# Optimization experiments

Measured on AMD Instinct MI355X. Metric: run time of the kernel, lower is better.

## Reference

```python
import jax, jax.numpy as jnp
import numpy as np

B, D_IN = 16384, 1024
N_DOM, EMB = 4, 16
H1, H2, H3 = 512, 256, 128
FH = 64
EPS = 1e-5


def setup_inputs() -> dict:
    key = jax.random.key(0)
    ks = jax.random.split(key, 32)
    s = 0.02
    def rn(k, shape):
        return jax.random.normal(k, shape, dtype=jnp.float32) * s
    inp = {
        "x": jax.random.normal(ks[0], (B, D_IN), dtype=jnp.float32),
        "domain_ids": jax.random.randint(ks[1], (B,), 0, N_DOM),
        # PartitionedNormalization params
        "pn_w": jnp.ones((N_DOM, D_IN), jnp.float32),
        "pn_b": jnp.zeros((N_DOM, D_IN), jnp.float32),
        # center net: D_IN->512->256->128
        "cW1": rn(ks[2], (D_IN, H1)), "cb1": jnp.zeros((H1,), jnp.float32),
        "cW2": rn(ks[3], (H1, H2)),  "cb2": jnp.zeros((H2,), jnp.float32),
        "cW3": rn(ks[4], (H2, H3)),  "cb3": jnp.zeros((H3,), jnp.float32),
        # domain-specific nets, stacked over domains
        "dW1": rn(ks[5], (N_DOM, D_IN, H1)), "db1": jnp.zeros((N_DOM, H1), jnp.float32),
        "dW2": rn(ks[6], (N_DOM, H1, H2)),  "db2": jnp.zeros((N_DOM, H2), jnp.float32),
        "dW3": rn(ks[7], (N_DOM, H2, H3)),  "db3": jnp.full((N_DOM, H3), 1.0, jnp.float32),  # domain_net_init_bias=1.0
        # final mlp: 128->64->1
        "fW1": rn(ks[8], (H3, FH)), "fb1": jnp.zeros((FH,), jnp.float32),
        "fW2": rn(ks[9], (FH, 1)),  "fb2": jnp.zeros((1,), jnp.float32),
        # domain embedding + auxiliary net: 16->32->1
        "dom_emb": rn(ks[10], (N_DOM, EMB)),
        "aW1": rn(ks[11], (EMB, 32)), "ab1": jnp.zeros((32,), jnp.float32),
        "aW2": rn(ks[12], (32, 1)),   "ab2": jnp.zeros((1,), jnp.float32),
    }
    return inp


def _forward(x, domain_ids, pn_w, pn_b,
             cW1, cb1, cW2, cb2, cW3, cb3,
             dW1, db1, dW2, db2, dW3, db3,
             fW1, fb1, fW2, fb2,
             dom_emb, aW1, ab1, aW2, ab2):
    # Partitioned normalization: per-sample layernorm over features,
    # domain-conditional affine (vectorized gather instead of python loop)
    mean = jnp.mean(x, axis=1, keepdims=True)
    var = jnp.mean(jnp.square(x - mean), axis=1, keepdims=True)  # unbiased=False
    norm = (x - mean) / jnp.sqrt(var + EPS)
    norm = norm * pn_w[domain_ids] + pn_b[domain_ids]  # (B, D_IN)

    # center net
    h = jax.nn.relu(norm @ cW1 + cb1)
    h = jax.nn.relu(h @ cW2 + cb2)
    h_center = h @ cW3 + cb3  # (B, H3)

    # domain-specific nets: compute all domains, then gather per-sample
    hd = jax.nn.relu(jnp.einsum('bi,dio->bdo', norm, dW1) + db1[None])   # (B,D,H1)
    hd = jax.nn.relu(jnp.einsum('bdi,dio->bdo', hd, dW2) + db2[None])    # (B,D,H2)
    hd = jnp.einsum('bdi,dio->bdo', hd, dW3) + db3[None]                 # (B,D,H3)
    h_domain = jnp.take_along_axis(hd, domain_ids[:, None, None], axis=1)[:, 0]  # (B,H3)

    h_fused = h_center * jnp.tanh(h_domain)

    main = jax.nn.relu(h_fused @ fW1 + fb1) @ fW2 + fb2  # (B,1)

    de = dom_emb[domain_ids]                              # (B,EMB)
    aux = jax.nn.relu(de @ aW1 + ab1) @ aW2 + ab2         # (B,1)

    return jax.nn.sigmoid(main + aux)


def reference(x, domain_ids, pn_w, pn_b,
              cW1, cb1, cW2, cb2, cW3, cb3,
              dW1, db1, dW2, db2, dW3, db3,
              fW1, fb1, fW2, fb2,
              dom_emb, aW1, ab1, aW2, ab2):
    return _forward(x, domain_ids, pn_w, pn_b,
                    cW1, cb1, cW2, cb2, cW3, cb3,
                    dW1, db1, dW2, db2, dW3, db3,
                    fW1, fb1, fW2, fb2,
                    dom_emb, aW1, ab1, aW2, ab2)
```

## Files before the change

kernel.cpp:

```cpp
#include <hip/hip_runtime.h>
#include <hip/hip_bf16.h>
#include <stdint.h>

#define NB   16384
#define DIN  1024
#define MPAD 16896

typedef __bf16 bf16;
typedef __bf16 v8bf __attribute__((ext_vector_type(8)));
typedef float  v4f  __attribute__((ext_vector_type(4)));

typedef __attribute__((address_space(1))) void* as1_ptr;
typedef __attribute__((address_space(3))) void* as3_ptr;

__device__ __forceinline__ void gl_lds16(const void* g, void* l) {
  __builtin_amdgcn_global_load_lds((as1_ptr)(g), (as3_ptr)(l), 16, 0, 0);
}

__device__ __forceinline__ unsigned short bfbits(float f) {
  bf16 h = (bf16)f;
  return __builtin_bit_cast(unsigned short, h);
}

__global__ __launch_bounds__(1024) void k_histscan_aux(
    const int* __restrict__ dom, int* __restrict__ pstart, int* __restrict__ cnt2,
    int* __restrict__ perm, float* __restrict__ aux,
    const float* __restrict__ dom_emb, const float* __restrict__ aW1,
    const float* __restrict__ ab1, const float* __restrict__ aW2,
    const float* __restrict__ ab2) {
  __shared__ int hist[4];
  int tid = threadIdx.x, lane = tid & 63;
  if (tid < 4) hist[tid] = 0;
  if (tid >= 8 && tid < 12) cnt2[tid - 8] = 0;
  for (int j = tid; j < MPAD; j += 1024) perm[j] = -1;
  __syncthreads();
  int c0 = 0, c1 = 0, c2 = 0, c3 = 0;
#pragma unroll
  for (int it = 0; it < 16; it++) {
    int d = dom[it * 1024 + tid];
    c0 += (d == 0); c1 += (d == 1); c2 += (d == 2); c3 += (d == 3);
  }
#pragma unroll
  for (int o = 32; o; o >>= 1) {
    c0 += __shfl_xor(c0, o, 64); c1 += __shfl_xor(c1, o, 64);
    c2 += __shfl_xor(c2, o, 64); c3 += __shfl_xor(c3, o, 64);
  }
  if (lane == 0) {
    atomicAdd(&hist[0], c0); atomicAdd(&hist[1], c1);
    atomicAdd(&hist[2], c2); atomicAdd(&hist[3], c3);
  }
  __syncthreads();
  if (tid == 0) {
    int p = 0;
    for (int d = 0; d < 4; d++) { pstart[d] = p; p += (hist[d] + 127) & ~127; }
    pstart[4] = p;
  }
  if (tid < 4) {
    float a = ab2[0];
    for (int j = 0; j < 32; j++) {
      float s = ab1[j];
      for (int i = 0; i < 16; i++) s += dom_emb[tid * 16 + i] * aW1[i * 32 + j];
      a += fmaxf(s, 0.f) * aW2[j];
    }
    aux[tid] = a;
  }
}

__global__ void k_assign(const int* __restrict__ dom, const int* __restrict__ pstart,
                         int* __restrict__ cnt2, int* __restrict__ perm,
                         int* __restrict__ rowpos) {
  int i = blockIdx.x * 256 + threadIdx.x;
  int lane = threadIdx.x & 63;
  int d = dom[i];
  unsigned long long ltmask = (1ull << lane) - 1ull;
#pragma unroll
  for (int dd = 0; dd < 4; dd++) {
    unsigned long long m = __ballot(d == dd);
    int c = __popcll(m);
    int base = 0;
    if (lane == 0 && c) base = atomicAdd(&cnt2[dd], c);
    base = __shfl(base, 0, 64);
    if (d == dd) {
      int pos = pstart[dd] + base + __popcll(m & ltmask);
      perm[pos] = i;
      rowpos[i] = pos;
    }
  }
}

__global__ __launch_bounds__(256) void k_ln(const float* __restrict__ x,
                                            const int* __restrict__ dom,
                                            const int* __restrict__ rowpos,
                                            const float* __restrict__ pn_w,
                                            const float* __restrict__ pn_b,
                                            bf16* __restrict__ norm) {
  int wv = threadIdx.x >> 6, lane = threadIdx.x & 63;
  int r = blockIdx.x * 4 + wv;
  const float* xr = x + (size_t)r * DIN;
  float4 v[4];
#pragma unroll
  for (int g = 0; g < 4; g++) v[g] = *(const float4*)(xr + g * 256 + lane * 4);
  float s = 0.f;
#pragma unroll
  for (int g = 0; g < 4; g++) s += v[g].x + v[g].y + v[g].z + v[g].w;
#pragma unroll
  for (int o = 32; o; o >>= 1) s += __shfl_xor(s, o, 64);
  float mean = s * (1.f / 1024.f);
  float q = 0.f;
#pragma unroll
  for (int g = 0; g < 4; g++) {
    float a = v[g].x - mean, b = v[g].y - mean, c = v[g].z - mean, e = v[g].w - mean;
    q += a * a + b * b + c * c + e * e;
  }
#pragma unroll
  for (int o = 32; o; o >>= 1) q += __shfl_xor(q, o, 64);
  float rstd = rsqrtf(q * (1.f / 1024.f) + 1e-5f);
  int d = dom[r];
  int pos = rowpos[r];
  const float* pw = pn_w + (size_t)d * DIN;
  const float* pb = pn_b + (size_t)d * DIN;
  bf16* orow = norm + (size_t)pos * DIN;
#pragma unroll
  for (int g = 0; g < 4; g++) {
    float4 w4 = *(const float4*)(pw + g * 256 + lane * 4);
    float4 b4 = *(const float4*)(pb + g * 256 + lane * 4);
    ushort4 o;
    o.x = bfbits((v[g].x - mean) * rstd * w4.x + b4.x);
    o.y = bfbits((v[g].y - mean) * rstd * w4.y + b4.y);
    o.z = bfbits((v[g].z - mean) * rstd * w4.z + b4.z);
    o.w = bfbits((v[g].w - mean) * rstd * w4.w + b4.w);
    *(ushort4*)(orow + g * 256 + lane * 4) = o;
  }
}

__global__ __launch_bounds__(256) void k_wt_all(
    const float* __restrict__ cW1, const float* __restrict__ cW2,
    const float* __restrict__ cW3, const float* __restrict__ dW1,
    const float* __restrict__ dW2, const float* __restrict__ dW3,
    const float* __restrict__ fW1,
    bf16* __restrict__ cW1t, bf16* __restrict__ cW2t, bf16* __restrict__ cW3t,
    bf16* __restrict__ dW1t, bf16* __restrict__ dW2t, bf16* __restrict__ dW3t,
    bf16* __restrict__ fW1t) {
  __shared__ float t[64 * 65];
  int bid = blockIdx.x;
  const float* src; bf16* dst; int K, N, tile;
  if (bid < 640) {
    K = 1024; N = 512; int m = bid >> 7; tile = bid & 127;
    src = m == 0 ? cW1 : dW1 + (size_t)(m - 1) * 524288;
    dst = m == 0 ? cW1t : dW1t + (size_t)(m - 1) * 524288;
  } else if (bid < 800) {
    K = 512; N = 256; int m = (bid - 640) >> 5; tile = (bid - 640) & 31;
    src = m == 0 ? cW2 : dW2 + (size_t)(m - 1) * 131072;
    dst = m == 0 ? cW2t : dW2t + (size_t)(m - 1) * 131072;
  } else if (bid < 840) {
    K = 256; N = 128; int m = (bid - 800) >> 3; tile = (bid - 800) & 7;
    src = m == 0 ? cW3 : dW3 + (size_t)(m - 1) * 32768;
    dst = m == 0 ? cW3t : dW3t + (size_t)(m - 1) * 32768;
  } else {
    K = 128; N = 64; tile = bid - 840;
    src = fW1; dst = fW1t;
  }
  int ntn = N >> 6;
  int k0 = (tile / ntn) << 6, n0 = (tile % ntn) << 6;
  int tid = threadIdx.x;
  int r = tid >> 2, c4 = (tid & 3) << 4;
#pragma unroll
  for (int j4 = 0; j4 < 4; j4++) {
    float4 v = *(const float4*)(src + (size_t)(k0 + r) * N + n0 + c4 + j4 * 4);
    t[r * 65 + c4 + j4 * 4 + 0] = v.x;
    t[r * 65 + c4 + j4 * 4 + 1] = v.y;
    t[r * 65 + c4 + j4 * 4 + 2] = v.z;
    t[r * 65 + c4 + j4 * 4 + 3] = v.w;
  }
  __syncthreads();
  int n = tid >> 2, kc = (tid & 3) << 4;
#pragma unroll
  for (int j4 = 0; j4 < 4; j4++) {
    ushort4 o;
    o.x = bfbits(t[(kc + j4 * 4 + 0) * 65 + n]);
    o.y = bfbits(t[(kc + j4 * 4 + 1) * 65 + n]);
    o.z = bfbits(t[(kc + j4 * 4 + 2) * 65 + n]);
    o.w = bfbits(t[(kc + j4 * 4 + 3) * 65 + n]);
    *(ushort4*)(dst + (size_t)(n0 + n) * K + k0 + kc + j4 * 4) = o;
  }
}

__global__ __launch_bounds__(256) void k_gemm(const bf16* __restrict__ A, int lda,
                                              int aoffc, int aoffd,
                                              const bf16* __restrict__ cWt,
                                              const bf16* __restrict__ dWt,
                                              const float* __restrict__ cb,
                                              const float* __restrict__ db,
                                              bf16* __restrict__ C, int Nh, int Kd,
                                              int relu, const int* __restrict__ pstart,
                                              int lognct) {
  __shared__ bf16 Al[128 * 64];
  __shared__ bf16 Bl[128 * 64];
  const int tid = threadIdx.x;
  const int wv = tid >> 6, lane = tid & 63;
  const int nct = 1 << lognct;
  const int T1 = nct << 7;
  int l = blockIdx.x, rt, ct;
  if (l < T1) {
    int t = l >> 3;
    ct = t & (nct - 1);
    rt = ((t >> lognct) << 3) | (l & 7);
  } else {
    int l2 = l - T1;
    rt = 128 + (l2 >> lognct);
    ct = l2 & (nct - 1);
  }
  const int row0 = rt * 128;
  int d = 0;
  if (row0 >= pstart[1]) d = 1;
  if (row0 >= pstart[2]) d = 2;
  if (row0 >= pstart[3]) d = 3;
  const int n0 = ct * 128;
  const bool isd = (n0 >= Nh);
  const bf16* Wt = isd ? dWt + ((size_t)d * Nh + (n0 - Nh)) * Kd : cWt + (size_t)n0 * Kd;
  const float* bias = isd ? db + d * Nh + (n0 - Nh) : cb + n0;
  const int aoff = isd ? aoffd : aoffc;
  const bf16* Ab = A + (size_t)row0 * lda + aoff;

  v4f acc[4][4];
#pragma unroll
  for (int i = 0; i < 4; i++)
#pragma unroll
    for (int j = 0; j < 4; j++) acc[i][j] = v4f{0.f, 0.f, 0.f, 0.f};

  const int wm = (wv >> 1) * 64, wn = (wv & 1) * 64;
  const int mrow = lane & 15, quad = lane >> 4;
  const int lrow = lane >> 3;
  const int lchk = lane & 7;
  const int ldc = 2 * Nh;

  for (int kt = 0; kt < Kd; kt += 64) {
#pragma unroll
    for (int p = 0; p < 4; p++) {
      int rbase = wv * 32 + p * 8;
      int r = rbase + lrow;
      int jg = lchk ^ (r & 7);
      gl_lds16(Ab + (size_t)r * lda + kt + jg * 8, &Al[rbase * 64]);
      gl_lds16(Wt + (size_t)r * Kd + kt + jg * 8, &Bl[rbase * 64]);
    }
    __syncthreads();
#pragma unroll
    for (int s = 0; s < 2; s++) {
      v8bf af[4], bfr[4];
#pragma unroll
      for (int mi = 0; mi < 4; mi++) {
        int m = wm + mi * 16 + mrow;
        int j = (s * 4 + quad) ^ (m & 7);
        af[mi] = *(const v8bf*)&Al[m * 64 + j * 8];
      }
#pragma unroll
      for (int ni = 0; ni < 4; ni++) {
        int n = wn + ni * 16 + mrow;
        int j = (s * 4 + quad) ^ (n & 7);
        bfr[ni] = *(const v8bf*)&Bl[n * 64 + j * 8];
      }
#pragma unroll
      for (int mi = 0; mi < 4; mi++)
#pragma unroll
        for (int ni = 0; ni < 4; ni++)
          acc[mi][ni] =
              __builtin_amdgcn_mfma_f32_16x16x32_bf16(af[mi], bfr[ni], acc[mi][ni], 0, 0, 0);
    }
    __syncthreads();
  }

  float bv[4];
#pragma unroll
  for (int ni = 0; ni < 4; ni++) bv[ni] = bias[wn + ni * 16 + mrow];
#pragma unroll
  for (int mi = 0; mi < 4; mi++) {
    int growb = row0 + wm + mi * 16 + quad * 4;
#pragma unroll
    for (int ni = 0; ni < 4; ni++) {
      int gcol = n0 + wn + ni * 16 + mrow;
#pragma unroll
      for (int r2 = 0; r2 < 4; r2++) {
        float v = acc[mi][ni][r2] + bv[ni];
        if (relu) v = fmaxf(v, 0.f);
        C[(size_t)(growb + r2) * ldc + gcol] = (bf16)v;
      }
    }
  }
}

__global__ __launch_bounds__(256) void k_gemm3(const bf16* __restrict__ A,
                                               const bf16* __restrict__ cW3t,
                                               const bf16* __restrict__ dW3t,
                                               const float* __restrict__ cb3,
                                               const float* __restrict__ db3,
                                               const bf16* __restrict__ fW1t,
                                               const float* __restrict__ fb1,
                                               const float* __restrict__ fW2,
                                               const float* __restrict__ fb2,
                                               const int* __restrict__ perm,
                                               const int* __restrict__ pstart,
                                               const float* __restrict__ aux,
                                               float* __restrict__ out) {
  __shared__ __align__(16) bf16 Al[64 * 64];
  __shared__ __align__(16) bf16 Bl[128 * 64];
  __shared__ __align__(16) bf16 fusedL[64 * 128];
  __shared__ __align__(16) bf16 fwB[64 * 128];
  const int tid = threadIdx.x, wv = tid >> 6, lane = tid & 63;
  const int row0 = blockIdx.x * 64;
  const int d = (row0 >= pstart[1]) + (row0 >= pstart[2]) + (row0 >= pstart[3]);
  const bf16* Ab = A + (size_t)row0 * 512;
  const int mrow = lane & 15, quad = lane >> 4, lrow = lane >> 3, lchk = lane & 7;
  const int wm = (wv >> 1) * 32, wn = (wv & 1) * 64;

  {
    int c = lane & 15, rsub = lane >> 4;
#pragma unroll
    for (int p = 0; p < 1; p++) {
      int rbase = wv * 16 + p * 4 * 4;
      (void)rbase;
    }
#pragma unroll
    for (int p = 0; p < 4; p++) {
      int rbase = wv * 16 + p * 4;
      int row = rbase + rsub;
      int g = (c & 8) | ((c ^ row) & 7);
      gl_lds16(fW1t + row * 128 + g * 8, &fwB[rbase * 128]);
    }
  }

  v4f accC[2][4], accD[2][4];
#pragma unroll
  for (int i = 0; i < 2; i++)
#pragma unroll
    for (int j = 0; j < 4; j++) { accC[i][j] = v4f{0.f,0.f,0.f,0.f}; accD[i][j] = v4f{0.f,0.f,0.f,0.f}; }

#pragma unroll
  for (int ph = 0; ph < 2; ph++) {
    const bf16* Wt = ph ? dW3t + (size_t)d * 32768 : cW3t;
    const int aoff = ph * 256;
    for (int kt = 0; kt < 256; kt += 64) {
#pragma unroll
      for (int p = 0; p < 2; p++) {
        int rbase = wv * 16 + p * 8;
        int r = rbase + lrow;
        int jg = lchk ^ (r & 7);
        gl_lds16(Ab + (size_t)r * 512 + aoff + kt + jg * 8, &Al[rbase * 64]);
      }
#pragma unroll
      for (int p = 0; p < 4; p++) {
        int rbase = wv * 32 + p * 8;
        int r = rbase + lrow;
        int jg = lchk ^ (r & 7);
        gl_lds16(Wt + (size_t)r * 256 + kt + jg * 8, &Bl[rbase * 64]);
      }
      __syncthreads();
#pragma unroll
      for (int s = 0; s < 2; s++) {
        v8bf af[2], bfr[4];
#pragma unroll
        for (int mi = 0; mi < 2; mi++) {
          int m = wm + mi * 16 + mrow;
          int j = (s * 4 + quad) ^ (m & 7);
          af[mi] = *(const v8bf*)&Al[m * 64 + j * 8];
        }
#pragma unroll
        for (int ni = 0; ni < 4; ni++) {
          int n = wn + ni * 16 + mrow;
          int j = (s * 4 + quad) ^ (n & 7);
          bfr[ni] = *(const v8bf*)&Bl[n * 64 + j * 8];
        }
        if (ph == 0) {
#pragma unroll
          for (int mi = 0; mi < 2; mi++)
#pragma unroll
            for (int ni = 0; ni < 4; ni++)
              accC[mi][ni] = __builtin_amdgcn_mfma_f32_16x16x32_bf16(af[mi], bfr[ni], accC[mi][ni], 0, 0, 0);
        } else {
#pragma unroll
          for (int mi = 0; mi < 2; mi++)
#pragma unroll
            for (int ni = 0; ni < 4; ni++)
              accD[mi][ni] = __builtin_amdgcn_mfma_f32_16x16x32_bf16(af[mi], bfr[ni], accD[mi][ni], 0, 0, 0);
        }
      }
      __syncthreads();
    }
  }

#pragma unroll
  for (int mi = 0; mi < 2; mi++) {
    int rowb = wm + mi * 16 + quad * 4;
#pragma unroll
    for (int ni = 0; ni < 4; ni++) {
      int col = wn + ni * 16 + mrow;
      float cbv = cb3[col];
      float dbv = db3[d * 128 + col];
      int jc = col >> 3, coff = col & 7;
#pragma unroll
      for (int r2 = 0; r2 < 4; r2++) {
        int rr = rowb + r2;
        float f = (accC[mi][ni][r2] + cbv) * tanhf(accD[mi][ni][r2] + dbv);
        int cs = (jc & 8) | ((jc ^ rr) & 7);
        fusedL[rr * 128 + cs * 8 + coff] = (bf16)f;
      }
    }
  }
  __syncthreads();

  float fb1v[4], fW2v[4];
#pragma unroll
  for (int nt = 0; nt < 4; nt++) {
    int col = nt * 16 + mrow;
    fb1v[nt] = fb1[col];
    fW2v[nt] = fW2[col];
  }
  v4f hacc[4];
#pragma unroll
  for (int nt = 0; nt < 4; nt++) hacc[nt] = v4f{0.f, 0.f, 0.f, 0.f};
  const int m = wv * 16 + mrow;
#pragma unroll
  for (int s = 0; s < 4; s++) {
    int j = s * 4 + quad;
    int ca = (j & 8) | ((j ^ m) & 7);
    v8bf af = *(const v8bf*)&fusedL[m * 128 + ca * 8];
#pragma unroll
    for (int nt = 0; nt < 4; nt++) {
      int n = nt * 16 + mrow;
      int cbk = (j & 8) | ((j ^ n) & 7);
      v8bf bfr = *(const v8bf*)&fwB[n * 128 + cbk * 8];
      hacc[nt] = __builtin_amdgcn_mfma_f32_16x16x32_bf16(af, bfr, hacc[nt], 0, 0, 0);
    }
  }
  float ys[4];
#pragma unroll
  for (int r2 = 0; r2 < 4; r2++) {
    float s = 0.f;
#pragma unroll
    for (int nt = 0; nt < 4; nt++) s += fmaxf(hacc[nt][r2] + fb1v[nt], 0.f) * fW2v[nt];
    ys[r2] = s;
  }
#pragma unroll
  for (int o = 1; o < 16; o <<= 1)
#pragma unroll
    for (int r2 = 0; r2 < 4; r2++) ys[r2] += __shfl_xor(ys[r2], o, 64);
  if (mrow == 0) {
    const float addc = fb2[0] + aux[d];
#pragma unroll
    for (int r2 = 0; r2 < 4; r2++) {
      int prow = row0 + wv * 16 + quad * 4 + r2;
      int orig = perm[prow];
      if (orig >= 0) out[orig] = 1.f / (1.f + expf(-(ys[r2] + addc)));
    }
  }
}

extern "C" void kernel_launch(void* const* d_in, const int* in_sizes, int n_in,
                              void* d_out, int out_size, void* d_ws, size_t ws_size,
                              hipStream_t stream) {
  (void)in_sizes; (void)n_in; (void)out_size; (void)ws_size;
  const float* x      = (const float*)d_in[0];
  const int*   dom    = (const int*)d_in[1];
  const float* pn_w   = (const float*)d_in[2];
  const float* pn_b   = (const float*)d_in[3];
  const float* cW1    = (const float*)d_in[4];
  const float* cb1    = (const float*)d_in[5];
  const float* cW2    = (const float*)d_in[6];
  const float* cb2    = (const float*)d_in[7];
  const float* cW3    = (const float*)d_in[8];
  const float* cb3    = (const float*)d_in[9];
  const float* dW1    = (const float*)d_in[10];
  const float* db1    = (const float*)d_in[11];
  const float* dW2    = (const float*)d_in[12];
  const float* db2    = (const float*)d_in[13];
  const float* dW3    = (const float*)d_in[14];
  const float* db3    = (const float*)d_in[15];
  const float* fW1    = (const float*)d_in[16];
  const float* fb1    = (const float*)d_in[17];
  const float* fW2    = (const float*)d_in[18];
  const float* fb2    = (const float*)d_in[19];
  const float* demb   = (const float*)d_in[20];
  const float* aW1    = (const float*)d_in[21];
  const float* ab1    = (const float*)d_in[22];
  const float* aW2    = (const float*)d_in[23];
  const float* ab2    = (const float*)d_in[24];
  float* out = (float*)d_out;

  char* w = (char*)d_ws;
  int*   cnt2   = (int*)(w + 16);
  int*   pstart = (int*)(w + 32);
  float* aux    = (float*)(w + 64);
  int*   perm   = (int*)(w + 256);
  int*   rowpos = (int*)(w + 67840);
  bf16*  bufA   = (bf16*)(w + 133376);
  bf16*  bufB   = (bf16*)(w + 34736384);
  bf16*  cW1t   = (bf16*)(w + 69339392);
  bf16*  cW2t   = (bf16*)(w + 70387968);
  bf16*  cW3t   = (bf16*)(w + 70650112);
  bf16*  dW1t   = (bf16*)(w + 70715648);
  bf16*  dW2t   = (bf16*)(w + 74909952);
  bf16*  dW3t   = (bf16*)(w + 75958528);
  bf16*  fW1t   = (bf16*)(w + 76220672);

  k_histscan_aux<<<1, 1024, 0, stream>>>(dom, pstart, cnt2, perm, aux,
                                         demb, aW1, ab1, aW2, ab2);
  k_assign<<<64, 256, 0, stream>>>(dom, pstart, cnt2, perm, rowpos);
  k_ln<<<4096, 256, 0, stream>>>(x, dom, rowpos, pn_w, pn_b, bufA);
  k_wt_all<<<842, 256, 0, stream>>>(cW1, cW2, cW3, dW1, dW2, dW3, fW1,
                                    cW1t, cW2t, cW3t, dW1t, dW2t, dW3t, fW1t);

  k_gemm<<<1056, 256, 0, stream>>>(bufA, 1024, 0, 0, cW1t, dW1t, cb1, db1,
                                   bufB, 512, 1024, 1, pstart, 3);
  k_gemm<<<528, 256, 0, stream>>>(bufB, 1024, 0, 512, cW2t, dW2t, cb2, db2,
                                  bufA, 256, 512, 1, pstart, 2);
  k_gemm3<<<264, 256, 0, stream>>>(bufA, cW3t, dW3t, cb3, db3, fW1t,
                                   fb1, fW2, fb2, perm, pstart, aux, out);
}
```

Before: 267.6 us.

## Switch activations and weights to FP8 MFMA and merge sort kernels

Converts normalized activations, intermediate hidden layers and the transposed weights from bf16 to fp8 (e4m3). Weights are scaled by 16 and outputs rescaled, and all three GEMM stages use fp8 MFMA, halving memory traffic and raising matrix throughput. Separately, the histogram and assignment kernels are merged into a single-block kernel using an LDS prefix scan, removing one launch and the atomics. The cost is much lower precision, which risks exceeding the accuracy tolerance.

Result: faster. 254.4 us (-4.9%).

```diff
diff --git a/kernel.cpp b/kernel.cpp
--- a/kernel.cpp
+++ b/kernel.cpp
@@ -9,6 +9,7 @@
 typedef __bf16 bf16;
 typedef __bf16 v8bf __attribute__((ext_vector_type(8)));
 typedef float  v4f  __attribute__((ext_vector_type(4)));
+typedef unsigned char u8;
 
 typedef __attribute__((address_space(1))) void* as1_ptr;
 typedef __attribute__((address_space(3))) void* as3_ptr;
@@ -22,38 +23,59 @@
   return __builtin_bit_cast(unsigned short, h);
 }
 
-__global__ __launch_bounds__(1024) void k_histscan_aux(
-    const int* __restrict__ dom, int* __restrict__ pstart, int* __restrict__ cnt2,
-    int* __restrict__ perm, float* __restrict__ aux,
+__device__ __forceinline__ unsigned short pk8(float a, float b) {
+  int u = __builtin_amdgcn_cvt_pk_fp8_f32(a, b, 0, false);
+  return (unsigned short)(u & 0xffff);
+}
+
+__global__ __launch_bounds__(1024) void k_sort(
+    const int* __restrict__ dom, int* __restrict__ pstart_g,
+    int* __restrict__ perm, int* __restrict__ rowpos, float* __restrict__ aux,
     const float* __restrict__ dom_emb, const float* __restrict__ aW1,
     const float* __restrict__ ab1, const float* __restrict__ aW2,
     const float* __restrict__ ab2) {
-  __shared__ int hist[4];
-  int tid = threadIdx.x, lane = tid & 63;
-  if (tid < 4) hist[tid] = 0;
-  if (tid >= 8 && tid < 12) cnt2[tid - 8] = 0;
+  __shared__ int sc0[1024], sc1[1024], sc2[1024], sc3[1024];
+  const int tid = threadIdx.x;
+  int dv[16];
+  int c0 = 0, c1 = 0, c2 = 0, c3 = 0;
+#pragma unroll
+  for (int it = 0; it < 16; it++) {
+    int d = dom[it * 1024 + tid];
+    dv[it] = d;
+    c0 += (d == 0); c1 += (d == 1); c2 += (d == 2); c3 += (d == 3);
+  }
+  sc0[tid] = c0; sc1[tid] = c1; sc2[tid] = c2; sc3[tid] = c3;
   for (int j = tid; j < MPAD; j += 1024) perm[j] = -1;
   __syncthreads();
-  int c0 = 0, c1 = 0, c2 = 0, c3 = 0;
+  for (int off = 1; off < 1024; off <<= 1) {
+    int v0 = (tid >= off) ? sc0[tid - off] : 0;
+    int v1 = (tid >= off) ? sc1[tid - off] : 0;
+    int v2 = (tid >= off) ? sc2[tid - off] : 0;
+    int v3 = (tid >= off) ? sc3[tid - off] : 0;
+    __syncthreads();
+    sc0[tid] += v0; sc1[tid] += v1; sc2[tid] += v2; sc3[tid] += v3;
+    __syncthreads();
+  }
+  const int t0 = sc0[1023], t1 = sc1[1023], t2 = sc2[1023];
+  const int s1 = (t0 + 127) & ~127;
+  const int s2 = s1 + ((t1 + 127) & ~127);
+  const int s3 = s2 + ((t2 + 127) & ~127);
+  int b0 = 0 + sc0[tid] - c0;
+  int b1 = s1 + sc1[tid] - c1;
+  int b2 = s2 + sc2[tid] - c2;
+  int b3 = s3 + sc3[tid] - c3;
 #pragma unroll
   for (int it = 0; it < 16; it++) {
-    int d = dom[it * 1024 + tid];
-    c0 += (d == 0); c1 += (d == 1); c2 += (d == 2); c3 += (d == 3);
-  }
-#pragma unroll
-  for (int o = 32; o; o >>= 1) {
-    c0 += __shfl_xor(c0, o, 64); c1 += __shfl_xor(c1, o, 64);
-    c2 += __shfl_xor(c2, o, 64); c3 += __shfl_xor(c3, o, 64);
-  }
-  if (lane == 0) {
-    atomicAdd(&hist[0], c0); atomicAdd(&hist[1], c1);
-    atomicAdd(&hist[2], c2); atomicAdd(&hist[3], c3);
-  }
-  __syncthreads();
+    int i = it * 1024 + tid;
+    int d = dv[it];
+    int pos = (d == 0) ? b0++ : ((d == 1) ? b1++ : ((d == 2) ? b2++ : b3++));
+    perm[pos] = i;
+    rowpos[i] = pos;
+  }
   if (tid == 0) {
-    int p = 0;
-    for (int d = 0; d < 4; d++) { pstart[d] = p; p += (hist[d] + 127) & ~127; }
-    pstart[4] = p;
+    int t3 = sc3[1023];
+    pstart_g[0] = 0; pstart_g[1] = s1; pstart_g[2] = s2; pstart_g[3] = s3;
+    pstart_g[4] = s3 + ((t3 + 127) & ~127);
   }
   if (tid < 4) {
     float a = ab2[0];
@@ -66,34 +88,12 @@
   }
 }
 
-__global__ void k_assign(const int* __restrict__ dom, const int* __restrict__ pstart,
-                         int* __restrict__ cnt2, int* __restrict__ perm,
-                         int* __restrict__ rowpos) {
-  int i = blockIdx.x * 256 + threadIdx.x;
-  int lane = threadIdx.x & 63;
-  int d = dom[i];
-  unsigned long long ltmask = (1ull << lane) - 1ull;
-#pragma unroll
-  for (int dd = 0; dd < 4; dd++) {
-    unsigned long long m = __ballot(d == dd);
-    int c = __popcll(m);
-    int base = 0;
-    if (lane == 0 && c) base = atomicAdd(&cnt2[dd], c);
-    base = __shfl(base, 0, 64);
-    if (d == dd) {
-      int pos = pstart[dd] + base + __popcll(m & ltmask);
-      perm[pos] = i;
-      rowpos[i] = pos;
-    }
-  }
-}
-
 __global__ __launch_bounds__(256) void k_ln(const float* __restrict__ x,
                                             const int* __restrict__ dom,
                                             const int* __restrict__ rowpos,
                                             const float* __restrict__ pn_w,
                                             const float* __restrict__ pn_b,
-                                            bf16* __restrict__ norm) {
+                                            u8* __restrict__ norm) {
   int wv = threadIdx.x >> 6, lane = threadIdx.x & 63;
   int r = blockIdx.x * 4 + wv;
   const float* xr = x + (size_t)r * DIN;
@@ -119,17 +119,18 @@
   int pos = rowpos[r];
   const float* pw = pn_w + (size_t)d * DIN;
   const float* pb = pn_b + (size_t)d * DIN;
-  bf16* orow = norm + (size_t)pos * DIN;
+  u8* orow = norm + (size_t)pos * DIN;
 #pragma unroll
   for (int g = 0; g < 4; g++) {
     float4 w4 = *(const float4*)(pw + g * 256 + lane * 4);
     float4 b4 = *(const float4*)(pb + g * 256 + lane * 4);
-    ushort4 o;
-    o.x = bfbits((v[g].x - mean) * rstd * w4.x + b4.x);
-    o.y = bfbits((v[g].y - mean) * rstd * w4.y + b4.y);
-    o.z = bfbits((v[g].z - mean) * rstd * w4.z + b4.z);
-    o.w = bfbits((v[g].w - mean) * rstd * w4.w + b4.w);
-    *(ushort4*)(orow + g * 256 + lane * 4) = o;
+    float f0 = (v[g].x - mean) * rstd * w4.x + b4.x;
+    float f1 = (v[g].y - mean) * rstd * w4.y + b4.y;
+    float f2 = (v[g].z - mean) * rstd * w4.z + b4.z;
+    float f3 = (v[g].w - mean) * rstd * w4.w + b4.w;
+    int u = __builtin_amdgcn_cvt_pk_fp8_f32(f0, f1, 0, false);
+    u = __builtin_amdgcn_cvt_pk_fp8_f32(f2, f3, u, true);
+    *(unsigned int*)(orow + g * 256 + lane * 4) = (unsigned int)u;
   }
 }
 
@@ -138,12 +139,12 @@
     const float* __restrict__ cW3, const float* __restrict__ dW1,
     const float* __restrict__ dW2, const float* __restrict__ dW3,
     const float* __restrict__ fW1,
-    bf16* __restrict__ cW1t, bf16* __restrict__ cW2t, bf16* __restrict__ cW3t,
-    bf16* __restrict__ dW1t, bf16* __restrict__ dW2t, bf16* __restrict__ dW3t,
+    u8* __restrict__ cW1t, u8* __restrict__ cW2t, u8* __restrict__ cW3t,
+    u8* __restrict__ dW1t, u8* __restrict__ dW2t, u8* __restrict__ dW3t,
     bf16* __restrict__ fW1t) {
   __shared__ float t[64 * 65];
   int bid = blockIdx.x;
-  const float* src; bf16* dst; int K, N, tile;
+  const float* src; u8* dst; int K, N, tile; bool isf = false;
   if (bid < 640) {
     K = 1024; N = 512; int m = bid >> 7; tile = bid & 127;
     src = m == 0 ? cW1 : dW1 + (size_t)(m - 1) * 524288;
@@ -157,8 +158,7 @@
     src = m == 0 ? cW3 : dW3 + (size_t)(m - 1) * 32768;
     dst = m == 0 ? cW3t : dW3t + (size_t)(m - 1) * 32768;
   } else {
-    K = 128; N = 64; tile = bid - 840;
-    src = fW1; dst = fW1t;
+    K = 128; N = 64; tile = bid - 840; src = fW1; dst = nullptr; isf = true;
   }
   int ntn = N >> 6;
   int k0 = (tile / ntn) << 6, n0 = (tile % ntn) << 6;
@@ -174,28 +174,41 @@
   }
   __syncthreads();
   int n = tid >> 2, kc = (tid & 3) << 4;
-#pragma unroll
-  for (int j4 = 0; j4 < 4; j4++) {
-    ushort4 o;
-    o.x = bfbits(t[(kc + j4 * 4 + 0) * 65 + n]);
-    o.y = bfbits(t[(kc + j4 * 4 + 1) * 65 + n]);
-    o.z = bfbits(t[(kc + j4 * 4 + 2) * 65 + n]);
-    o.w = bfbits(t[(kc + j4 * 4 + 3) * 65 + n]);
-    *(ushort4*)(dst + (size_t)(n0 + n) * K + k0 + kc + j4 * 4) = o;
-  }
-}
-
-__global__ __launch_bounds__(256) void k_gemm(const bf16* __restrict__ A, int lda,
+  if (!isf) {
+#pragma unroll
+    for (int j4 = 0; j4 < 4; j4++) {
+      float v0 = t[(kc + j4 * 4 + 0) * 65 + n] * 16.f;
+      float v1 = t[(kc + j4 * 4 + 1) * 65 + n] * 16.f;
+      float v2 = t[(kc + j4 * 4 + 2) * 65 + n] * 16.f;
+      float v3 = t[(kc + j4 * 4 + 3) * 65 + n] * 16.f;
+      int u = __builtin_amdgcn_cvt_pk_fp8_f32(v0, v1, 0, false);
+      u = __builtin_amdgcn_cvt_pk_fp8_f32(v2, v3, u, true);
+      *(unsigned int*)(dst + (size_t)(n0 + n) * K + k0 + kc + j4 * 4) = (unsigned int)u;
+    }
+  } else {
+#pragma unroll
+    for (int j4 = 0; j4 < 4; j4++) {
+      ushort4 o;
+      o.x = bfbits(t[(kc + j4 * 4 + 0) * 65 + n]);
+      o.y = bfbits(t[(kc + j4 * 4 + 1) * 65 + n]);
+      o.z = bfbits(t[(kc + j4 * 4 + 2) * 65 + n]);
+      o.w = bfbits(t[(kc + j4 * 4 + 3) * 65 + n]);
+      *(ushort4*)(fW1t + (size_t)(n0 + n) * K + k0 + kc + j4 * 4) = o;
+    }
+  }
+}
+
+__global__ __launch_bounds__(256) void k_gemm(const u8* __restrict__ A, int lda,
                                               int aoffc, int aoffd,
-                                              const bf16* __restrict__ cWt,
-                                              const bf16* __restrict__ dWt,
+                                              const u8* __restrict__ cWt,
+                                              const u8* __restrict__ dWt,
                                               const float* __restrict__ cb,
                                               const float* __restrict__ db,
-                                              bf16* __restrict__ C, int Nh, int Kd,
+                                              u8* __restrict__ C, int Nh, int Kd,
                                               int relu, const int* __restrict__ pstart,
                                               int lognct) {
-  __shared__ bf16 Al[128 * 64];
-  __shared__ bf16 Bl[128 * 64];
+  __shared__ __align__(16) u8 Al[128 * 64];
+  __shared__ __align__(16) u8 Bl[128 * 64];
   const int tid = threadIdx.x;
   const int wv = tid >> 6, lane = tid & 63;
   const int nct = 1 << lognct;
@@ -217,10 +230,10 @@
   if (row0 >= pstart[3]) d = 3;
   const int n0 = ct * 128;
   const bool isd = (n0 >= Nh);
-  const bf16* Wt = isd ? dWt + ((size_t)d * Nh + (n0 - Nh)) * Kd : cWt + (size_t)n0 * Kd;
+  const u8* Wt = isd ? dWt + ((size_t)d * Nh + (n0 - Nh)) * Kd : cWt + (size_t)n0 * Kd;
   const float* bias = isd ? db + d * Nh + (n0 - Nh) : cb + n0;
   const int aoff = isd ? aoffd : aoffc;
-  const bf16* Ab = A + (size_t)row0 * lda + aoff;
+  const u8* Ab = A + (size_t)row0 * lda + aoff;
 
   v4f acc[4][4];
 #pragma unroll
@@ -230,41 +243,43 @@
 
   const int wm = (wv >> 1) * 64, wn = (wv & 1) * 64;
   const int mrow = lane & 15, quad = lane >> 4;
-  const int lrow = lane >> 3;
-  const int lchk = lane & 7;
+  const int lrow = lane >> 2;
+  const int lchk = lane & 3;
   const int ldc = 2 * Nh;
 
   for (int kt = 0; kt < Kd; kt += 64) {
 #pragma unroll
-    for (int p = 0; p < 4; p++) {
-      int rbase = wv * 32 + p * 8;
+    for (int p = 0; p < 2; p++) {
+      int rbase = wv * 32 + p * 16;
       int r = rbase + lrow;
-      int jg = lchk ^ (r & 7);
-      gl_lds16(Ab + (size_t)r * lda + kt + jg * 8, &Al[rbase * 64]);
-      gl_lds16(Wt + (size_t)r * Kd + kt + jg * 8, &Bl[rbase * 64]);
+      int jg = lchk ^ (r & 3);
+      gl_lds16(Ab + (size_t)r * lda + kt + jg * 16, &Al[rbase * 64]);
+      gl_lds16(Wt + (size_t)r * Kd + kt + jg * 16, &Bl[rbase * 64]);
     }
     __syncthreads();
 #pragma unroll
     for (int s = 0; s < 2; s++) {
-      v8bf af[4], bfr[4];
+      long af[4], bfr[4];
 #pragma unroll
       for (int mi = 0; mi < 4; mi++) {
         int m = wm + mi * 16 + mrow;
-        int j = (s * 4 + quad) ^ (m & 7);
-        af[mi] = *(const v8bf*)&Al[m * 64 + j * 8];
+        int jc = s * 2 + (quad >> 1);
+        int js = jc ^ (m & 3);
+        af[mi] = *(const long*)&Al[m * 64 + js * 16 + (quad & 1) * 8];
       }
 #pragma unroll
       for (int ni = 0; ni < 4; ni++) {
         int n = wn + ni * 16 + mrow;
-        int j = (s * 4 + quad) ^ (n & 7);
-        bfr[ni] = *(const v8bf*)&Bl[n * 64 + j * 8];
+        int jc = s * 2 + (quad >> 1);
+        int js = jc ^ (n & 3);
+        bfr[ni] = *(const long*)&Bl[n * 64 + js * 16 + (quad & 1) * 8];
       }
 #pragma unroll
       for (int mi = 0; mi < 4; mi++)
 #pragma unroll
         for (int ni = 0; ni < 4; ni++)
           acc[mi][ni] =
-              __builtin_amdgcn_mfma_f32_16x16x32_bf16(af[mi], bfr[ni], acc[mi][ni], 0, 0, 0);
+              __builtin_amdgcn_mfma_f32_16x16x32_fp8_fp8(af[mi], bfr[ni], acc[mi][ni], 0, 0, 0);
     }
     __syncthreads();
   }
@@ -280,17 +295,19 @@
       int gcol = n0 + wn + ni * 16 + mrow;
 #pragma unroll
       for (int r2 = 0; r2 < 4; r2++) {
-        float v = acc[mi][ni][r2] + bv[ni];
+        float v = acc[mi][ni][r2] * 0.0625f + bv[ni];
         if (relu) v = fmaxf(v, 0.f);
-        C[(size_t)(growb + r2) * ldc + gcol] = (bf16)v;
-      }
-    }
-  }
-}
-
-__global__ __launch_bounds__(256) void k_gemm3(const bf16* __restrict__ A,
-                                               const bf16* __restrict__ cW3t,
-                                               const bf16* __restrict__ dW3t,
+        float g = __shfl_xor(v, 1, 64);
+        if (!(mrow & 1))
+          *(unsigned short*)(C + (size_t)(growb + r2) * ldc + gcol) = pk8(v, g);
+      }
+    }
+  }
+}
+
+__global__ __launch_bounds__(256) void k_gemm3(const u8* __restrict__ A,
+                                               const u8* __restrict__ cW3t,
+                                               const u8* __restrict__ dW3t,
                                                const float* __restrict__ cb3,
                                                const float* __restrict__ db3,
                                                const bf16* __restrict__ fW1t,
@@ -301,24 +318,20 @@
                                                const int* __restrict__ pstart,
                                                const float* __restrict__ aux,
                                                float* __restrict__ out) {
-  __shared__ __align__(16) bf16 Al[64 * 64];
-  __shared__ __align__(16) bf16 Bl[128 * 64];
+  __shared__ __align__(16) u8 Al[64 * 64];
+  __shared__ __align__(16) u8 Bl[128 * 64];
   __shared__ __align__(16) bf16 fusedL[64 * 128];
   __shared__ __align__(16) bf16 fwB[64 * 128];
   const int tid = threadIdx.x, wv = tid >> 6, lane = tid & 63;
   const int row0 = blockIdx.x * 64;
   const int d = (row0 >= pstart[1]) + (row0 >= pstart[2]) + (row0 >= pstart[3]);
-  const bf16* Ab = A + (size_t)row0 * 512;
-  const int mrow = lane & 15, quad = lane >> 4, lrow = lane >> 3, lchk = lane & 7;
+  const u8* Ab = A + (size_t)row0 * 512;
+  const int mrow = lane & 15, quad = lane >> 4;
+  const int lrow = lane >> 2, lchk = lane & 3;
   const int wm = (wv >> 1) * 32, wn = (wv & 1) * 64;
 
   {
     int c = lane & 15, rsub = lane >> 4;
-#pragma unroll
-    for (int p = 0; p < 1; p++) {
-      int rbase = wv * 16 + p * 4 * 4;
-      (void)rbase;
-    }
 #pragma unroll
     for (int p = 0; p < 4; p++) {
       int rbase = wv * 16 + p * 4;
@@ -336,51 +349,52 @@
 
 #pragma unroll
   for (int ph = 0; ph < 2; ph++) {
-    const bf16* Wt = ph ? dW3t + (size_t)d * 32768 : cW3t;
+    const u8* Wt = ph ? dW3t + (size_t)d * 32768 : cW3t;
     const int aoff = ph * 256;
     for (int kt = 0; kt < 256; kt += 64) {
+      {
+        int rbase = wv * 16;
+        int r = rbase + lrow;
+        int jg = lchk ^ (r & 3);
+        gl_lds16(Ab + (size_t)r * 512 + aoff + kt + jg * 16, &Al[rbase * 64]);
+      }
 #pragma unroll
       for (int p = 0; p < 2; p++) {
-        int rbase = wv * 16 + p * 8;
+        int rbase = wv * 32 + p * 16;
         int r = rbase + lrow;
-        int jg = lchk ^ (r & 7);
-        gl_lds16(Ab + (size_t)r * 512 + aoff + kt + jg * 8, &Al[rbase * 64]);
-      }
-#pragma unroll
-      for (int p = 0; p < 4; p++) {
-        int rbase = wv * 32 + p * 8;
-        int r = rbase + lrow;
-        int jg = lchk ^ (r & 7);
-        gl_lds16(Wt + (size_t)r * 256 + kt + jg * 8, &Bl[rbase * 64]);
+        int jg = lchk ^ (r & 3);
+        gl_lds16(Wt + (size_t)r * 256 + kt + jg * 16, &Bl[rbase * 64]);
       }
       __syncthreads();
 #pragma unroll
       for (int s = 0; s < 2; s++) {
-        v8bf af[2], bfr[4];
+        long af[2], bfr[4];
 #pragma unroll
         for (int mi = 0; mi < 2; mi++) {
           int m = wm + mi * 16 + mrow;
-          int j = (s * 4 + quad) ^ (m & 7);
-          af[mi] = *(const v8bf*)&Al[m * 64 + j * 8];
+          int jc = s * 2 + (quad >> 1);
+          int js = jc ^ (m & 3);
+          af[mi] = *(const long*)&Al[m * 64 + js * 16 + (quad & 1) * 8];
         }
 #pragma unroll
         for (int ni = 0; ni < 4; ni++) {
           int n = wn + ni * 16 + mrow;
-          int j = (s * 4 + quad) ^ (n & 7);
-          bfr[ni] = *(const v8bf*)&Bl[n * 64 + j * 8];
+          int jc = s * 2 + (quad >> 1);
+          int js = jc ^ (n & 3);
+          bfr[ni] = *(const long*)&Bl[n * 64 + js * 16 + (quad & 1) * 8];
         }
         if (ph == 0) {
 #pragma unroll
           for (int mi = 0; mi < 2; mi++)
 #pragma unroll
             for (int ni = 0; ni < 4; ni++)
-              accC[mi][ni] = __builtin_amdgcn_mfma_f32_16x16x32_bf16(af[mi], bfr[ni], accC[mi][ni], 0, 0, 0);
+              accC[mi][ni] = __builtin_amdgcn_mfma_f32_16x16x32_fp8_fp8(af[mi], bfr[ni], accC[mi][ni], 0, 0, 0);
         } else {
 #pragma unroll
           for (int mi = 0; mi < 2; mi++)
 #pragma unroll
             for (int ni = 0; ni < 4; ni++)
-              accD[mi][ni] = __builtin_amdgcn_mfma_f32_16x16x32_bf16(af[mi], bfr[ni], accD[mi][ni], 0, 0, 0);
+              accD[mi][ni] = __builtin_amdgcn_mfma_f32_16x16x32_fp8_fp8(af[mi], bfr[ni], accD[mi][ni], 0, 0, 0);
         }
       }
       __syncthreads();
@@ -399,7 +413,7 @@
 #pragma unroll
       for (int r2 = 0; r2 < 4; r2++) {
         int rr = rowb + r2;
-        float f = (accC[mi][ni][r2] + cbv) * tanhf(accD[mi][ni][r2] + dbv);
+        float f = (accC[mi][ni][r2] * 0.0625f + cbv) * tanhf(accD[mi][ni][r2] * 0.0625f + dbv);
         int cs = (jc & 8) | ((jc ^ rr) & 7);
         fusedL[rr * 128 + cs * 8 + coff] = (bf16)f;
       }
@@ -486,24 +500,22 @@
   float* out = (float*)d_out;
 
   char* w = (char*)d_ws;
-  int*   cnt2   = (int*)(w + 16);
   int*   pstart = (int*)(w + 32);
   float* aux    = (float*)(w + 64);
   int*   perm   = (int*)(w + 256);
   int*   rowpos = (int*)(w + 67840);
-  bf16*  bufA   = (bf16*)(w + 133376);
-  bf16*  bufB   = (bf16*)(w + 34736384);
-  bf16*  cW1t   = (bf16*)(w + 69339392);
-  bf16*  cW2t   = (bf16*)(w + 70387968);
-  bf16*  cW3t   = (bf16*)(w + 70650112);
-  bf16*  dW1t   = (bf16*)(w + 70715648);
-  bf16*  dW2t   = (bf16*)(w + 74909952);
-  bf16*  dW3t   = (bf16*)(w + 75958528);
-  bf16*  fW1t   = (bf16*)(w + 76220672);
-
-  k_histscan_aux<<<1, 1024, 0, stream>>>(dom, pstart, cnt2, perm, aux,
-                                         demb, aW1, ab1, aW2, ab2);
-  k_assign<<<64, 256, 0, stream>>>(dom, pstart, cnt2, perm, rowpos);
+  u8*    bufA   = (u8*)(w + 133376);
+  u8*    bufB   = (u8*)(w + 17434880);
+  u8*    cW1t   = (u8*)(w + 34736384);
+  u8*    cW2t   = (u8*)(w + 35260672);
+  u8*    cW3t   = (u8*)(w + 35391744);
+  u8*    dW1t   = (u8*)(w + 35424512);
+  u8*    dW2t   = (u8*)(w + 37521664);
+  u8*    dW3t   = (u8*)(w + 38045952);
+  bf16*  fW1t   = (bf16*)(w + 38177024);
+
+  k_sort<<<1, 1024, 0, stream>>>(dom, pstart, perm, rowpos, aux,
+                                 demb, aW1, ab1, aW2, ab2);
   k_ln<<<4096, 256, 0, stream>>>(x, dom, rowpos, pn_w, pn_b, bufA);
   k_wt_all<<<842, 256, 0, stream>>>(cW1, cW2, cW3, dW1, dW2, dW3, fW1,
                                     cW1t, cW2t, cW3t, dW1t, dW2t, dW3t, fW1t);
```
